# Kernel optimization log

Hardware: AMD Instinct MI355X
Metric: run time of the kernel (lower is better)

## Reference

```python
import jax, jax.numpy as jnp
import numpy as np

N_NODES = 100000
N_EDGES = 600000
D = 128          # input_dim
H = 256          # hidden_dim


def setup_inputs() -> dict:
    key = jax.random.key(0)
    k_emb, k_edge, k_w1, k_w2 = jax.random.split(key, 4)
    emd_all = jax.random.normal(k_emb, (N_NODES, D), dtype=jnp.float32)
    edge_index = jax.random.randint(k_edge, (N_EDGES, 2), 0, N_NODES, dtype=jnp.int32)
    # Linear(2*D, H) and Linear(H, 1); scale like torch default init ~ 1/sqrt(fan_in)
    W1 = jax.random.normal(k_w1, (2 * D, H), dtype=jnp.float32) / np.sqrt(2 * D)
    b1 = jnp.zeros((H,), dtype=jnp.float32)
    W2 = jax.random.normal(k_w2, (H, 1), dtype=jnp.float32) / np.sqrt(H)
    b2 = jnp.zeros((1,), dtype=jnp.float32)
    return {"emd_all": emd_all, "edge_index": edge_index,
            "W1": W1, "b1": b1, "W2": W2, "b2": b2}


def reference(emd_all, edge_index, W1, b1, W2, b2):
    # Gather source / destination node embeddings and concatenate: [E, 2*D]
    src = emd_all[edge_index[:, 0]]
    dst = emd_all[edge_index[:, 1]]
    edge_embeds = jnp.concatenate([src, dst], axis=-1)
    # 2-layer MLP classifier + sigmoid: [E, 1]
    h = jax.nn.relu(edge_embeds @ W1 + b1)
    logits = h @ W2 + b2
    link_predictions = jax.nn.sigmoid(logits)
    return link_predictions
```

## Files before the change

### kernel.cpp

```cpp
#include <hip/hip_runtime.h>
#include <hip/hip_bf16.h>

#define N_EDGES_C 600000
#define D_C 128

typedef __attribute__((ext_vector_type(8))) short short8;
typedef __attribute__((ext_vector_type(4))) float f32x4;

__device__ inline unsigned short f2bf(float f) {
    unsigned int u = __builtin_bit_cast(unsigned int, f);
    u += 0x7FFF + ((u >> 16) & 1);
    return (unsigned short)(u >> 16);
}

__device__ inline unsigned int pk2bf(float lo, float hi) {
    return (unsigned int)f2bf(lo) | ((unsigned int)f2bf(hi) << 16);
}

__global__ void prep_w1f(const float* __restrict__ W1, unsigned short* __restrict__ w1f) {
    int o = blockIdx.x * 256 + threadIdx.x;
    int j    = o & 7;
    int lane = (o >> 3) & 63;
    int kk   = (o >> 9) & 7;
    int nf   = o >> 12;
    int k = kk * 32 + (lane >> 4) * 8 + j;
    int n = nf * 16 + (lane & 15);
    w1f[o] = f2bf(W1[k * 256 + n]);
}

__global__ __launch_bounds__(256, 4) void edge_mlp(
    const float* __restrict__ emd,
    const int* __restrict__ eidx,
    const unsigned short* __restrict__ w1f,
    const float* __restrict__ b1,
    const float* __restrict__ W2,
    const float* __restrict__ b2,
    float* __restrict__ out)
{
    __shared__ unsigned char smem[32768];

    const int t    = threadIdx.x;
    const int lane = t & 63;
    const int wv   = t >> 6;
    const int rr_c = lane & 15;
    const int lg   = lane >> 4;

    const int e0 = blockIdx.x * 64;

    {
        const int kk = lane >> 3;
        const int kl = (lane >> 1) & 3;
        const int lanepart = kk * 1024 + kl * 256 + (lane & 1) * 8;
        const int f4 = lane & 31;

        #pragma unroll
        for (int p = 0; p < 16; ++p) {
            const int row = p * 4 + wv;
            const int2 ep = *reinterpret_cast<const int2*>(eidx + (size_t)(e0 + row) * 2);
            const int idx = (lane < 32) ? ep.x : ep.y;
            const float4 v = *reinterpret_cast<const float4*>(emd + (size_t)idx * D_C + f4 * 4);
            uint2 pk;
            pk.x = pk2bf(v.x, v.y);
            pk.y = pk2bf(v.z, v.w);
            const int m  = row >> 4;
            const int rr = row & 15;
            *reinterpret_cast<uint2*>(smem + (m * 8192 + lanepart + ((rr ^ kk) << 4))) = pk;
        }
    }
    __syncthreads();

    f32x4 acc[4][4];
    #pragma unroll
    for (int m = 0; m < 4; ++m)
        #pragma unroll
        for (int n4 = 0; n4 < 4; ++n4) acc[m][n4] = (f32x4){0.f, 0.f, 0.f, 0.f};

    #pragma unroll
    for (int kk = 0; kk < 8; ++kk) {
        const int alow = ((lane & 48) | ((lane & 15) ^ kk)) << 4;
        short8 a[4];
        #pragma unroll
        for (int m = 0; m < 4; ++m)
            a[m] = *reinterpret_cast<const short8*>(smem + (m * 8 + kk) * 1024 + alow);
        #pragma unroll
        for (int n4 = 0; n4 < 4; ++n4) {
            short8 b = *reinterpret_cast<const short8*>(
                w1f + ((size_t)((wv * 4 + n4) * 8 + kk) * 64 + lane) * 8);
            #pragma unroll
            for (int m = 0; m < 4; ++m)
                acc[m][n4] = __builtin_amdgcn_mfma_f32_16x16x32_bf16(a[m], b, acc[m][n4], 0, 0, 0);
        }
    }

    float pr[4][4];
    #pragma unroll
    for (int m = 0; m < 4; ++m)
        #pragma unroll
        for (int g = 0; g < 4; ++g) pr[m][g] = 0.f;

    #pragma unroll
    for (int n4 = 0; n4 < 4; ++n4) {
        int n = wv * 64 + n4 * 16 + rr_c;
        float b1v = b1[n];
        float w2v = W2[n];
        #pragma unroll
        for (int m = 0; m < 4; ++m)
            #pragma unroll
            for (int g = 0; g < 4; ++g) {
                float h = acc[m][n4][g] + b1v;
                h = h > 0.f ? h : 0.f;
                pr[m][g] += h * w2v;
            }
    }

    #pragma unroll
    for (int msk = 8; msk >= 1; msk >>= 1) {
        #pragma unroll
        for (int m = 0; m < 4; ++m)
            #pragma unroll
            for (int g = 0; g < 4; ++g)
                pr[m][g] += __shfl_xor(pr[m][g], msk, 64);
    }

    __syncthreads();
    float* partial = (float*)smem;

    if (rr_c == 0) {
        #pragma unroll
        for (int m = 0; m < 4; ++m)
            #pragma unroll
            for (int g = 0; g < 4; ++g)
                partial[wv * 64 + m * 16 + lg * 4 + g] = pr[m][g];
    }
    __syncthreads();

    if (t < 64) {
        float s = partial[t] + partial[64 + t] + partial[128 + t] + partial[192 + t] + b2[0];
        out[e0 + t] = 1.0f / (1.0f + __expf(-s));
    }
}

extern "C" void kernel_launch(void* const* d_in, const int* in_sizes, int n_in,
                              void* d_out, int out_size, void* d_ws, size_t ws_size,
                              hipStream_t stream) {
    const float* emd  = (const float*)d_in[0];
    const int*   eidx = (const int*)d_in[1];
    const float* W1   = (const float*)d_in[2];
    const float* b1   = (const float*)d_in[3];
    const float* W2   = (const float*)d_in[4];
    const float* b2   = (const float*)d_in[5];
    float* out = (float*)d_out;
    unsigned short* w1f = (unsigned short*)d_ws;

    prep_w1f<<<256, 256, 0, stream>>>(W1, w1f);

    const int nblocks = N_EDGES_C / 64;
    edge_mlp<<<nblocks, 256, 0, stream>>>(emd, eidx, w1f, b1, W2, b2, out);
}
```

Measured before the change: 161.9 us.

## Make edge MLP persistent with double-buffered LDS prefetch of next tile

```diff
diff --git a/kernel.cpp b/kernel.cpp
--- a/kernel.cpp
+++ b/kernel.cpp
@@ -3,6 +3,8 @@
 
 #define N_EDGES_C 600000
 #define D_C 128
+#define NTILES 9375
+#define GRIDB 1024
 
 typedef __attribute__((ext_vector_type(8))) short short8;
 typedef __attribute__((ext_vector_type(4))) float f32x4;
@@ -28,7 +30,7 @@
     w1f[o] = f2bf(W1[k * 256 + n]);
 }
 
-__global__ __launch_bounds__(256, 4) void edge_mlp(
+__global__ __launch_bounds__(256, 2) void edge_mlp(
     const float* __restrict__ emd,
     const int* __restrict__ eidx,
     const unsigned short* __restrict__ w1f,
@@ -37,7 +39,8 @@
     const float* __restrict__ b2,
     float* __restrict__ out)
 {
-    __shared__ unsigned char smem[32768];
+    extern __shared__ unsigned char smem[];
+    float* partial = (float*)(smem + 65536);
 
     const int t    = threadIdx.x;
     const int lane = t & 63;
@@ -45,98 +48,138 @@
     const int rr_c = lane & 15;
     const int lg   = lane >> 4;
 
-    const int e0 = blockIdx.x * 64;
-
-    {
-        const int kk = lane >> 3;
-        const int kl = (lane >> 1) & 3;
-        const int lanepart = kk * 1024 + kl * 256 + (lane & 1) * 8;
-        const int f4 = lane & 31;
-
-        #pragma unroll
-        for (int p = 0; p < 16; ++p) {
-            const int row = p * 4 + wv;
-            const int2 ep = *reinterpret_cast<const int2*>(eidx + (size_t)(e0 + row) * 2);
-            const int idx = (lane < 32) ? ep.x : ep.y;
-            const float4 v = *reinterpret_cast<const float4*>(emd + (size_t)idx * D_C + f4 * 4);
-            uint2 pk;
-            pk.x = pk2bf(v.x, v.y);
-            pk.y = pk2bf(v.z, v.w);
-            const int m  = row >> 4;
-            const int rr = row & 15;
-            *reinterpret_cast<uint2*>(smem + (m * 8192 + lanepart + ((rr ^ kk) << 4))) = pk;
-        }
-    }
-    __syncthreads();
-
-    f32x4 acc[4][4];
-    #pragma unroll
-    for (int m = 0; m < 4; ++m)
-        #pragma unroll
-        for (int n4 = 0; n4 < 4; ++n4) acc[m][n4] = (f32x4){0.f, 0.f, 0.f, 0.f};
-
-    #pragma unroll
-    for (int kk = 0; kk < 8; ++kk) {
-        const int alow = ((lane & 48) | ((lane & 15) ^ kk)) << 4;
-        short8 a[4];
-        #pragma unroll
-        for (int m = 0; m < 4; ++m)
-            a[m] = *reinterpret_cast<const short8*>(smem + (m * 8 + kk) * 1024 + alow);
-        #pragma unroll
-        for (int n4 = 0; n4 < 4; ++n4) {
-            short8 b = *reinterpret_cast<const short8*>(
-                w1f + ((size_t)((wv * 4 + n4) * 8 + kk) * 64 + lane) * 8);
-            #pragma unroll
-            for (int m = 0; m < 4; ++m)
-                acc[m][n4] = __builtin_amdgcn_mfma_f32_16x16x32_bf16(a[m], b, acc[m][n4], 0, 0, 0);
-        }
-    }
-
-    float pr[4][4];
-    #pragma unroll
-    for (int m = 0; m < 4; ++m)
-        #pragma unroll
-        for (int g = 0; g < 4; ++g) pr[m][g] = 0.f;
-
+    const int L    = lane & 31;
+    const int kkw  = (lane >> 5) * 4 + (L >> 3);
+    const int klw  = (L >> 1) & 3;
+    const int wbase = kkw * 1024 + klw * 256 + (lane & 1) * 8;
+    const int wxor  = (kkw ^ (klw << 1)) & 7;
+
+    const int klsh = (lane >> 4) << 1;
+
+    float b1v[4], w2v[4];
     #pragma unroll
     for (int n4 = 0; n4 < 4; ++n4) {
         int n = wv * 64 + n4 * 16 + rr_c;
-        float b1v = b1[n];
-        float w2v = W2[n];
+        b1v[n4] = b1[n];
+        w2v[n4] = W2[n];
+    }
+    const float b2v = b2[0];
+
+    int tile = blockIdx.x;
+
+    {
+        uint2 pk[16];
+        #pragma unroll
+        for (int p = 0; p < 16; ++p) {
+            const int row = p * 4 + wv;
+            const int2 ep = *reinterpret_cast<const int2*>(eidx + (size_t)(tile * 64 + row) * 2);
+            const int idx = (lane < 32) ? ep.x : ep.y;
+            const float4 v = *reinterpret_cast<const float4*>(emd + (size_t)idx * D_C + L * 4);
+            pk[p].x = pk2bf(v.x, v.y);
+            pk[p].y = pk2bf(v.z, v.w);
+        }
+        #pragma unroll
+        for (int p = 0; p < 16; ++p) {
+            const int row = p * 4 + wv;
+            *reinterpret_cast<uint2*>(smem +
+                ((row >> 4) * 8192 + wbase + (((row & 15) ^ wxor) << 4))) = pk[p];
+        }
+    }
+
+    int cur = 0;
+    for (; tile < NTILES; tile += GRIDB) {
+        const int ntile = tile + GRIDB;
+        const bool has_next = ntile < NTILES;
+
+        uint2 pk[16];
+        if (has_next) {
+            #pragma unroll
+            for (int p = 0; p < 16; ++p) {
+                const int row = p * 4 + wv;
+                const int2 ep = *reinterpret_cast<const int2*>(eidx + (size_t)(ntile * 64 + row) * 2);
+                const int idx = (lane < 32) ? ep.x : ep.y;
+                const float4 v = *reinterpret_cast<const float4*>(emd + (size_t)idx * D_C + L * 4);
+                pk[p].x = pk2bf(v.x, v.y);
+                pk[p].y = pk2bf(v.z, v.w);
+            }
+        }
+
+        __syncthreads();
+
+        const unsigned char* buf = smem + cur * 32768;
+        f32x4 acc[4][4];
         #pragma unroll
         for (int m = 0; m < 4; ++m)
             #pragma unroll
-            for (int g = 0; g < 4; ++g) {
-                float h = acc[m][n4][g] + b1v;
-                h = h > 0.f ? h : 0.f;
-                pr[m][g] += h * w2v;
+            for (int n4 = 0; n4 < 4; ++n4) acc[m][n4] = (f32x4){0.f, 0.f, 0.f, 0.f};
+
+        #pragma unroll
+        for (int kk = 0; kk < 8; ++kk) {
+            const int aoff = ((lane & 48) | (rr_c ^ ((kk ^ klsh) & 7))) << 4;
+            short8 a[4];
+            #pragma unroll
+            for (int m = 0; m < 4; ++m)
+                a[m] = *reinterpret_cast<const short8*>(buf + (m * 8 + kk) * 1024 + aoff);
+            #pragma unroll
+            for (int n4 = 0; n4 < 4; ++n4) {
+                short8 b = *reinterpret_cast<const short8*>(
+                    w1f + ((size_t)((wv * 4 + n4) * 8 + kk) * 64 + lane) * 8);
+                #pragma unroll
+                for (int m = 0; m < 4; ++m)
+                    acc[m][n4] = __builtin_amdgcn_mfma_f32_16x16x32_bf16(a[m], b, acc[m][n4], 0, 0, 0);
             }
-    }
-
-    #pragma unroll
-    for (int msk = 8; msk >= 1; msk >>= 1) {
+        }
+
+        float pr[4][4];
         #pragma unroll
         for (int m = 0; m < 4; ++m)
             #pragma unroll
-            for (int g = 0; g < 4; ++g)
-                pr[m][g] += __shfl_xor(pr[m][g], msk, 64);
-    }
-
-    __syncthreads();
-    float* partial = (float*)smem;
-
-    if (rr_c == 0) {
-        #pragma unroll
-        for (int m = 0; m < 4; ++m)
-            #pragma unroll
-            for (int g = 0; g < 4; ++g)
-                partial[wv * 64 + m * 16 + lg * 4 + g] = pr[m][g];
-    }
-    __syncthreads();
-
-    if (t < 64) {
-        float s = partial[t] + partial[64 + t] + partial[128 + t] + partial[192 + t] + b2[0];
-        out[e0 + t] = 1.0f / (1.0f + __expf(-s));
+            for (int g = 0; g < 4; ++g) pr[m][g] = 0.f;
+
+        #pragma unroll
+        for (int n4 = 0; n4 < 4; ++n4) {
+            #pragma unroll
+            for (int m = 0; m < 4; ++m)
+                #pragma unroll
+                for (int g = 0; g < 4; ++g) {
+                    float h = acc[m][n4][g] + b1v[n4];
+                    h = h > 0.f ? h : 0.f;
+                    pr[m][g] += h * w2v[n4];
+                }
+        }
+        #pragma unroll
+        for (int msk = 8; msk >= 1; msk >>= 1) {
+            #pragma unroll
+            for (int m = 0; m < 4; ++m)
+                #pragma unroll
+                for (int g = 0; g < 4; ++g)
+                    pr[m][g] += __shfl_xor(pr[m][g], msk, 64);
+        }
+        if (rr_c == 0) {
+            #pragma unroll
+            for (int m = 0; m < 4; ++m)
+                #pragma unroll
+                for (int g = 0; g < 4; ++g)
+                    partial[wv * 64 + m * 16 + lg * 4 + g] = pr[m][g];
+        }
+
+        if (has_next) {
+            unsigned char* nbuf = smem + (cur ^ 1) * 32768;
+            #pragma unroll
+            for (int p = 0; p < 16; ++p) {
+                const int row = p * 4 + wv;
+                *reinterpret_cast<uint2*>(nbuf +
+                    ((row >> 4) * 8192 + wbase + (((row & 15) ^ wxor) << 4))) = pk[p];
+            }
+        }
+
+        __syncthreads();
+
+        if (t < 64) {
+            float s = partial[t] + partial[64 + t] + partial[128 + t] + partial[192 + t] + b2v;
+            out[(size_t)tile * 64 + t] = 1.0f / (1.0f + __expf(-s));
+        }
+        cur ^= 1;
     }
 }
 
@@ -154,6 +197,6 @@
 
     prep_w1f<<<256, 256, 0, stream>>>(W1, w1f);
 
-    const int nblocks = N_EDGES_C / 64;
-    edge_mlp<<<nblocks, 256, 0, stream>>>(emd, eidx, w1f, b1, W2, b2, out);
-}
+    const size_t lds_bytes = 2 * 32768 + 256 * sizeof(float);
+    edge_mlp<<<GRIDB, 256, lds_bytes, stream>>>(emd, eidx, w1f, b1, W2, b2, out);
+}
```

Result: slower. 216.7 us (+33.8%).
